# Optimization experiments

Hardware: AMD Instinct MI355X
Metric: run time of the kernel (lower is better)

## Reference

```python
import jax, jax.numpy as jnp
import numpy as np

N = 50000
E = 1600000
R = 4
D_IN = 128
D_OUT = 128


def setup_inputs() -> dict:
    key = jax.random.key(0)
    ks = jax.random.split(key, 7)
    x = jax.random.normal(ks[0], (N, D_IN), dtype=jnp.float32)
    vals = jax.random.normal(ks[1], (R, E), dtype=jnp.float32) * (1.0 / 32.0)
    weight = jax.random.normal(ks[2], (D_IN, D_OUT), dtype=jnp.float32) * (1.0 / np.sqrt(D_IN))
    filt = jax.random.uniform(ks[3], (R * N, 1), dtype=jnp.float32, minval=0.9, maxval=1.1)
    bias = jnp.zeros((D_OUT,), dtype=jnp.float32)
    rows = jax.random.randint(ks[4], (R, E), 0, N, dtype=jnp.int32)
    cols = jax.random.randint(ks[5], (R, E), 0, N, dtype=jnp.int32)
    return {"x": x, "vals": vals, "weight": weight, "filt": filt,
            "bias": bias, "rows": rows, "cols": cols}


def _spmm(rows, cols, vals, h, n):
    # sparse [n,n] @ dense [n,d] via gather + segment_sum
    return jax.ops.segment_sum(vals[:, None] * h[cols], rows, num_segments=n)


def reference(x, vals, weight, filt, bias, rows, cols):
    n = x.shape[0]
    h = x @ weight                                    # [N, out]
    # cat(d_list, dim=0) @ h  ->  stack of D_i @ h, i.e. [R, N, out]
    y = jax.vmap(lambda r, c, v: _spmm(r, c, v, h, n))(rows, cols, vals)
    y = filt.reshape(rows.shape[0], n, 1) * y         # elementwise wavelet filter
    # cat(d_list, dim=1) @ y  ->  sum_i D_i @ y_i
    out = jax.vmap(lambda r, c, v, yy: _spmm(r, c, v, yy, n))(rows, cols, vals, y).sum(axis=0)
    return out + bias
```

## Files before the change

### kernel.cpp

```cpp
#include <hip/hip_runtime.h>

#define N_NODES 50000
#define N_EDGES 1600000
#define R_WAV 4
#define D 128
#define NB 391
#define CHUNK 4096
#define NPBLK ((N_EDGES + CHUNK - 1) / CHUNK)
#define MAXB 4800

typedef unsigned int u32;
typedef unsigned short u16;

static __device__ inline u16 f2bf(float f) {
    u32 u = __float_as_uint(f);
    u = (u + 0x7FFFu + ((u >> 16) & 1u)) >> 16;
    return (u16)u;
}
static __device__ inline float bf_lo(u32 u) { return __uint_as_float(u << 16); }
static __device__ inline float bf_hi(u32 u) { return __uint_as_float(u & 0xFFFF0000u); }

__global__ __launch_bounds__(128) void gemm_xw(const float* __restrict__ x,
                                               const float* __restrict__ W,
                                               u16* __restrict__ h) {
    __shared__ float xs[4 * 128];
    const int j = threadIdx.x;
    const int row0 = blockIdx.x * 4;
    for (int t = j; t < 512; t += 128) xs[t] = x[(size_t)row0 * D + t];
    __syncthreads();
    float a0 = 0.f, a1 = 0.f, a2 = 0.f, a3 = 0.f;
#pragma unroll 8
    for (int k = 0; k < 128; ++k) {
        const float w = W[k * D + j];
        a0 += xs[k] * w;
        a1 += xs[128 + k] * w;
        a2 += xs[256 + k] * w;
        a3 += xs[384 + k] * w;
    }
    h[(size_t)(row0 + 0) * D + j] = f2bf(a0);
    h[(size_t)(row0 + 1) * D + j] = f2bf(a1);
    h[(size_t)(row0 + 2) * D + j] = f2bf(a2);
    h[(size_t)(row0 + 3) * D + j] = f2bf(a3);
}

__global__ __launch_bounds__(256) void bucket_hist_all(const int* __restrict__ rows_all,
                                                       int* __restrict__ cnt4) {
    __shared__ int lh[NB];
    const int r = blockIdx.y;
    const int* rows = rows_all + (size_t)r * N_EDGES;
    int* cnt = cnt4 + r * NB;
    const int tid = threadIdx.x;
    for (int i = tid; i < NB; i += 256) lh[i] = 0;
    __syncthreads();
    const int e0 = blockIdx.x * CHUNK;
    const int e1 = min(e0 + CHUNK, N_EDGES);
    for (int i = e0 + tid; i < e1; i += 256) atomicAdd(&lh[rows[i] >> 7], 1);
    __syncthreads();
    for (int i = tid; i < NB; i += 256) {
        const int c = lh[i];
        if (c) atomicAdd(&cnt[i], c);
    }
}

__global__ __launch_bounds__(512) void scan_buckets_all(const int* __restrict__ cnt4,
                                                        int* __restrict__ bptr4,
                                                        int* __restrict__ bcur4) {
    __shared__ int sa[512], sb[512];
    const int r = blockIdx.x;
    const int* cnt = cnt4 + r * NB;
    int* bptr = bptr4 + r * (NB + 1);
    int* bcur = bcur4 + r * NB;
    const int tid = threadIdx.x;
    const int v = (tid < NB) ? cnt[tid] : 0;
    sa[tid] = v;
    int* cur = sa;
    int* nxt = sb;
    for (int d = 1; d < 512; d <<= 1) {
        __syncthreads();
        int t = cur[tid];
        if (tid >= d) t += cur[tid - d];
        nxt[tid] = t;
        int* tmp = cur; cur = nxt; nxt = tmp;
    }
    __syncthreads();
    const int excl = cur[tid] - v;
    if (tid <= NB) bptr[tid] = excl;
    if (tid < NB) bcur[tid] = excl;
}

__global__ __launch_bounds__(256) void partition_kernel(const int* __restrict__ rows,
                                                        const int* __restrict__ cols,
                                                        const float* __restrict__ vals,
                                                        int* __restrict__ bcur,
                                                        int2* __restrict__ cv) {
    __shared__ int lh[NB], lptr[NB], lcur[NB], lbase[NB];
    __shared__ int sa[256], sb[256];
    __shared__ int2 st[CHUNK];
    const int tid = threadIdx.x;
    for (int i = tid; i < NB; i += 256) lh[i] = 0;
    __syncthreads();
    const int e0 = blockIdx.x * CHUNK;
    const int e1 = min(e0 + CHUNK, N_EDGES);
    const int cnt = e1 - e0;
    for (int i = e0 + tid; i < e1; i += 256) atomicAdd(&lh[rows[i] >> 7], 1);
    __syncthreads();
    const int p0 = (2 * tid < NB) ? lh[2 * tid] : 0;
    const int p1 = (2 * tid + 1 < NB) ? lh[2 * tid + 1] : 0;
    sa[tid] = p0 + p1;
    int* cur = sa;
    int* nxt = sb;
    for (int d = 1; d < 256; d <<= 1) {
        __syncthreads();
        int t = cur[tid];
        if (tid >= d) t += cur[tid - d];
        nxt[tid] = t;
        int* tmp = cur; cur = nxt; nxt = tmp;
    }
    __syncthreads();
    const int pe = cur[tid] - (p0 + p1);
    if (2 * tid < NB)     { lptr[2 * tid] = pe;           lcur[2 * tid] = pe; }
    if (2 * tid + 1 < NB) { lptr[2 * tid + 1] = pe + p0;  lcur[2 * tid + 1] = pe + p0; }
    __syncthreads();
    for (int i = e0 + tid; i < e1; i += 256) {
        const int row = rows[i];
        const int b = row >> 7;
        const int pos = atomicAdd(&lcur[b], 1);
        st[pos] = make_int2((int)(((u32)row << 16) | (u32)cols[i]), __float_as_int(vals[i]));
    }
    __syncthreads();
    for (int b = tid; b < NB; b += 256) {
        const int c = lh[b];
        int gb = 0;
        if (c) gb = atomicAdd(&bcur[b], c);
        lbase[b] = gb - lptr[b];
    }
    __syncthreads();
    for (int i = tid; i < cnt; i += 256) {
        const int2 e = st[i];
        const int b = (int)((u32)e.x >> 23);
        cv[lbase[b] + i] = e;
    }
}

__global__ __launch_bounds__(256) void bucket_csr(const int* __restrict__ bptr,
                                                  const int2* __restrict__ cv,
                                                  u32* __restrict__ cv4,
                                                  int* __restrict__ row_ptr) {
    __shared__ int lh[128], lexcl[128], lcur[128];
    __shared__ u32 st[MAXB];
    const int b = blockIdx.x;
    const int s = bptr[b], e1 = bptr[b + 1];
    const int cnt = e1 - s;
    const int tid = threadIdx.x;
    if (tid < 128) lh[tid] = 0;
    __syncthreads();
    for (int i = s + tid; i < e1; i += 256)
        atomicAdd(&lh[((u32)cv[i].x >> 16) & 127u], 1);
    __syncthreads();
    if (tid < 64) {
        const int p0 = lh[2 * tid], p1 = lh[2 * tid + 1];
        int ssum = p0 + p1;
#pragma unroll
        for (int d = 1; d < 64; d <<= 1) {
            const int t = __shfl_up(ssum, d, 64);
            if (tid >= d) ssum += t;
        }
        const int pe = ssum - (p0 + p1);
        lexcl[2 * tid] = pe;          lcur[2 * tid] = pe;
        lexcl[2 * tid + 1] = pe + p0; lcur[2 * tid + 1] = pe + p0;
    }
    __syncthreads();
    for (int i = s + tid; i < e1; i += 256) {
        const int2 E = cv[i];
        const int lr = (int)(((u32)E.x >> 16) & 127u);
        const int pos = atomicAdd(&lcur[lr], 1);
        if (pos < MAXB)
            st[pos] = ((u32)f2bf(__int_as_float(E.y)) << 16) | ((u32)E.x & 0xFFFFu);
    }
    __syncthreads();
    const int wb = (cnt < MAXB) ? cnt : MAXB;
    for (int i = tid; i < wb; i += 256) cv4[s + i] = st[i];
    if (tid < 128) {
        const int row = (b << 7) + tid;
        if (row < N_NODES) row_ptr[row] = s + lexcl[tid];
    }
    if (b == 0 && tid == 0) row_ptr[N_NODES] = N_EDGES;
}

__global__ __launch_bounds__(256) void spmm1(const int* __restrict__ row_ptr,
                                             const u32* __restrict__ cvp,
                                             const u32* __restrict__ h2,
                                             const float* __restrict__ filt_r,
                                             u32* __restrict__ y2) {
    const int row = __builtin_amdgcn_readfirstlane(blockIdx.x * 4 + (threadIdx.x >> 6));
    const int lane = threadIdx.x & 63;
    const int half = lane >> 5;
    const int l = lane & 31;
    int e = row_ptr[row];
    const int end = row_ptr[row + 1];
    float a0 = 0.f, a1 = 0.f, a2 = 0.f, a3 = 0.f;
    float b0 = 0.f, b1 = 0.f, b2 = 0.f, b3 = 0.f;
    for (; e + 8 <= end; e += 8) {
        const u32 c0 = cvp[e], c1 = cvp[e + 1], c2 = cvp[e + 2], c3 = cvp[e + 3];
        const u32 c4 = cvp[e + 4], c5 = cvp[e + 5], c6 = cvp[e + 6], c7 = cvp[e + 7];
        const u32 uA = half ? c1 : c0;
        const u32 uB = half ? c3 : c2;
        const u32 uC = half ? c5 : c4;
        const u32 uD = half ? c7 : c6;
        const uint2 gA = *(const uint2*)(h2 + (uA & 0xFFFFu) * 64 + 2 * l);
        const uint2 gB = *(const uint2*)(h2 + (uB & 0xFFFFu) * 64 + 2 * l);
        const uint2 gC = *(const uint2*)(h2 + (uC & 0xFFFFu) * 64 + 2 * l);
        const uint2 gD = *(const uint2*)(h2 + (uD & 0xFFFFu) * 64 + 2 * l);
        const float vA = __uint_as_float(uA & 0xFFFF0000u);
        const float vB = __uint_as_float(uB & 0xFFFF0000u);
        const float vC = __uint_as_float(uC & 0xFFFF0000u);
        const float vD = __uint_as_float(uD & 0xFFFF0000u);
        a0 += vA * bf_lo(gA.x); a1 += vA * bf_hi(gA.x);
        a2 += vA * bf_lo(gA.y); a3 += vA * bf_hi(gA.y);
        b0 += vB * bf_lo(gB.x); b1 += vB * bf_hi(gB.x);
        b2 += vB * bf_lo(gB.y); b3 += vB * bf_hi(gB.y);
        a0 += vC * bf_lo(gC.x); a1 += vC * bf_hi(gC.x);
        a2 += vC * bf_lo(gC.y); a3 += vC * bf_hi(gC.y);
        b0 += vD * bf_lo(gD.x); b1 += vD * bf_hi(gD.x);
        b2 += vD * bf_lo(gD.y); b3 += vD * bf_hi(gD.y);
    }
    for (; e < end; e += 2) {
        const u32 c0 = cvp[e];
        const u32 c1 = (e + 1 < end) ? cvp[e + 1] : 0u;
        const u32 uA = half ? c1 : c0;
        const uint2 gA = *(const uint2*)(h2 + (uA & 0xFFFFu) * 64 + 2 * l);
        const float vA = __uint_as_float(uA & 0xFFFF0000u);
        a0 += vA * bf_lo(gA.x); a1 += vA * bf_hi(gA.x);
        a2 += vA * bf_lo(gA.y); a3 += vA * bf_hi(gA.y);
    }
    a0 += b0; a1 += b1; a2 += b2; a3 += b3;
    a0 += __shfl_xor(a0, 32, 64);
    a1 += __shfl_xor(a1, 32, 64);
    a2 += __shfl_xor(a2, 32, 64);
    a3 += __shfl_xor(a3, 32, 64);
    const float f = filt_r[row];
    if (half == 0) {
        uint2 o;
        o.x = (u32)f2bf(f * a0) | ((u32)f2bf(f * a1) << 16);
        o.y = (u32)f2bf(f * a2) | ((u32)f2bf(f * a3) << 16);
        *(uint2*)(y2 + (size_t)row * 64 + 2 * l) = o;
    }
}

template <bool FIRST>
__global__ __launch_bounds__(256) void spmm2(const int* __restrict__ row_ptr,
                                             const u32* __restrict__ cvp,
                                             const u32* __restrict__ y2,
                                             const float* __restrict__ bias,
                                             float* __restrict__ out) {
    const int row = __builtin_amdgcn_readfirstlane(blockIdx.x * 4 + (threadIdx.x >> 6));
    const int lane = threadIdx.x & 63;
    const int half = lane >> 5;
    const int l = lane & 31;
    int e = row_ptr[row];
    const int end = row_ptr[row + 1];
    float a0 = 0.f, a1 = 0.f, a2 = 0.f, a3 = 0.f;
    float b0 = 0.f, b1 = 0.f, b2 = 0.f, b3 = 0.f;
    for (; e + 8 <= end; e += 8) {
        const u32 c0 = cvp[e], c1 = cvp[e + 1], c2 = cvp[e + 2], c3 = cvp[e + 3];
        const u32 c4 = cvp[e + 4], c5 = cvp[e + 5], c6 = cvp[e + 6], c7 = cvp[e + 7];
        const u32 uA = half ? c1 : c0;
        const u32 uB = half ? c3 : c2;
        const u32 uC = half ? c5 : c4;
        const u32 uD = half ? c7 : c6;
        const uint2 gA = *(const uint2*)(y2 + (uA & 0xFFFFu) * 64 + 2 * l);
        const uint2 gB = *(const uint2*)(y2 + (uB & 0xFFFFu) * 64 + 2 * l);
        const uint2 gC = *(const uint2*)(y2 + (uC & 0xFFFFu) * 64 + 2 * l);
        const uint2 gD = *(const uint2*)(y2 + (uD & 0xFFFFu) * 64 + 2 * l);
        const float vA = __uint_as_float(uA & 0xFFFF0000u);
        const float vB = __uint_as_float(uB & 0xFFFF0000u);
        const float vC = __uint_as_float(uC & 0xFFFF0000u);
        const float vD = __uint_as_float(uD & 0xFFFF0000u);
        a0 += vA * bf_lo(gA.x); a1 += vA * bf_hi(gA.x);
        a2 += vA * bf_lo(gA.y); a3 += vA * bf_hi(gA.y);
        b0 += vB * bf_lo(gB.x); b1 += vB * bf_hi(gB.x);
        b2 += vB * bf_lo(gB.y); b3 += vB * bf_hi(gB.y);
        a0 += vC * bf_lo(gC.x); a1 += vC * bf_hi(gC.x);
        a2 += vC * bf_lo(gC.y); a3 += vC * bf_hi(gC.y);
        b0 += vD * bf_lo(gD.x); b1 += vD * bf_hi(gD.x);
        b2 += vD * bf_lo(gD.y); b3 += vD * bf_hi(gD.y);
    }
    for (; e < end; e += 2) {
        const u32 c0 = cvp[e];
        const u32 c1 = (e + 1 < end) ? cvp[e + 1] : 0u;
        const u32 uA = half ? c1 : c0;
        const uint2 gA = *(const uint2*)(y2 + (uA & 0xFFFFu) * 64 + 2 * l);
        const float vA = __uint_as_float(uA & 0xFFFF0000u);
        a0 += vA * bf_lo(gA.x); a1 += vA * bf_hi(gA.x);
        a2 += vA * bf_lo(gA.y); a3 += vA * bf_hi(gA.y);
    }
    a0 += b0; a1 += b1; a2 += b2; a3 += b3;
    a0 += __shfl_xor(a0, 32, 64);
    a1 += __shfl_xor(a1, 32, 64);
    a2 += __shfl_xor(a2, 32, 64);
    a3 += __shfl_xor(a3, 32, 64);
    if (half == 0) {
        float* op = out + (size_t)row * D + 4 * l;
        if (FIRST) {
            const float4 bb = *(const float4*)(bias + 4 * l);
            *(float4*)op = make_float4(a0 + bb.x, a1 + bb.y, a2 + bb.z, a3 + bb.w);
        } else {
            const float4 cc = *(const float4*)op;
            *(float4*)op = make_float4(cc.x + a0, cc.y + a1, cc.z + a2, cc.w + a3);
        }
    }
}

extern "C" void kernel_launch(void* const* d_in, const int* in_sizes, int n_in,
                              void* d_out, int out_size, void* d_ws, size_t ws_size,
                              hipStream_t stream) {
    const float* x    = (const float*)d_in[0];
    const float* vals = (const float*)d_in[1];
    const float* W    = (const float*)d_in[2];
    const float* filt = (const float*)d_in[3];
    const float* bias = (const float*)d_in[4];
    const int*   rows = (const int*)d_in[5];
    const int*   cols = (const int*)d_in[6];
    float* out = (float*)d_out;

    char* ws = (char*)d_ws;
    u16*  h       = (u16*)(ws);
    u32*  y2      = (u32*)(ws + 12800000);
    int2* cv8     = (int2*)(ws + 25600000);
    u32*  cv4     = (u32*)(ws + 38400000);
    int*  row_ptr = (int*)(ws + 44800512);
    int*  cnt4    = (int*)(ws + 45000576);
    int*  bptr4   = (int*)(ws + 45006976);
    int*  bcur4   = (int*)(ws + 45013376);

    gemm_xw<<<N_NODES / 4, 128, 0, stream>>>(x, W, h);

    hipMemsetAsync(cnt4, 0, 4 * NB * sizeof(int), stream);
    bucket_hist_all<<<dim3(NPBLK, R_WAV), 256, 0, stream>>>(rows, cnt4);
    scan_buckets_all<<<R_WAV, 512, 0, stream>>>(cnt4, bptr4, bcur4);

    for (int r = 0; r < R_WAV; ++r) {
        const int*   rows_r = rows + (size_t)r * N_EDGES;
        const int*   cols_r = cols + (size_t)r * N_EDGES;
        const float* vals_r = vals + (size_t)r * N_EDGES;
        const float* filt_r = filt + (size_t)r * N_NODES;

        partition_kernel<<<NPBLK, 256, 0, stream>>>(rows_r, cols_r, vals_r,
                                                    bcur4 + r * NB, cv8);
        bucket_csr<<<NB, 256, 0, stream>>>(bptr4 + r * (NB + 1), cv8, cv4, row_ptr);
        spmm1<<<N_NODES / 4, 256, 0, stream>>>(row_ptr, cv4, (const u32*)h, filt_r, y2);
        if (r == 0)
            spmm2<true><<<N_NODES / 4, 256, 0, stream>>>(row_ptr, cv4, y2, bias, out);
        else
            spmm2<false><<<N_NODES / 4, 256, 0, stream>>>(row_ptr, cv4, y2, bias, out);
    }
}
```

Baseline: 734.2 us.

## Batch CSR build and first SpMM across wavelets; deterministic partition offsets

```diff
diff --git a/kernel.cpp b/kernel.cpp
--- a/kernel.cpp
+++ b/kernel.cpp
@@ -8,6 +8,7 @@
 #define CHUNK 4096
 #define NPBLK ((N_EDGES + CHUNK - 1) / CHUNK)
 #define MAXB 4800
+#define RP_STRIDE 50016
 
 typedef unsigned int u32;
 typedef unsigned short u16;
@@ -23,53 +24,74 @@
 __global__ __launch_bounds__(128) void gemm_xw(const float* __restrict__ x,
                                                const float* __restrict__ W,
                                                u16* __restrict__ h) {
-    __shared__ float xs[4 * 128];
     const int j = threadIdx.x;
-    const int row0 = blockIdx.x * 4;
-    for (int t = j; t < 512; t += 128) xs[t] = x[(size_t)row0 * D + t];
-    __syncthreads();
-    float a0 = 0.f, a1 = 0.f, a2 = 0.f, a3 = 0.f;
-#pragma unroll 8
+    const int row0 = blockIdx.x * 16;
+    const float* xr = x + (size_t)row0 * D;
+    float acc[16];
+#pragma unroll
+    for (int r = 0; r < 16; ++r) acc[r] = 0.f;
+#pragma unroll 4
     for (int k = 0; k < 128; ++k) {
         const float w = W[k * D + j];
-        a0 += xs[k] * w;
-        a1 += xs[128 + k] * w;
-        a2 += xs[256 + k] * w;
-        a3 += xs[384 + k] * w;
-    }
-    h[(size_t)(row0 + 0) * D + j] = f2bf(a0);
-    h[(size_t)(row0 + 1) * D + j] = f2bf(a1);
-    h[(size_t)(row0 + 2) * D + j] = f2bf(a2);
-    h[(size_t)(row0 + 3) * D + j] = f2bf(a3);
+#pragma unroll
+        for (int r = 0; r < 16; ++r) acc[r] += xr[r * D + k] * w;
+    }
+#pragma unroll
+    for (int r = 0; r < 16; ++r) h[(size_t)(row0 + r) * D + j] = f2bf(acc[r]);
 }
 
 __global__ __launch_bounds__(256) void bucket_hist_all(const int* __restrict__ rows_all,
-                                                       int* __restrict__ cnt4) {
+                                                       int* __restrict__ hist,
+                                                       int* __restrict__ deg) {
     __shared__ int lh[NB];
     const int r = blockIdx.y;
     const int* rows = rows_all + (size_t)r * N_EDGES;
-    int* cnt = cnt4 + r * NB;
+    int* dg = deg + (size_t)r * N_NODES;
     const int tid = threadIdx.x;
     for (int i = tid; i < NB; i += 256) lh[i] = 0;
     __syncthreads();
     const int e0 = blockIdx.x * CHUNK;
     const int e1 = min(e0 + CHUNK, N_EDGES);
-    for (int i = e0 + tid; i < e1; i += 256) atomicAdd(&lh[rows[i] >> 7], 1);
-    __syncthreads();
-    for (int i = tid; i < NB; i += 256) {
-        const int c = lh[i];
-        if (c) atomicAdd(&cnt[i], c);
-    }
+    for (int i = e0 + tid; i < e1; i += 256) {
+        const int row = rows[i];
+        atomicAdd(&lh[row >> 7], 1);
+        atomicAdd(&dg[row], 1);
+    }
+    __syncthreads();
+    int* hc = hist + ((size_t)r * NPBLK + blockIdx.x) * NB;
+    for (int i = tid; i < NB; i += 256) hc[i] = lh[i];
+}
+
+__global__ __launch_bounds__(512) void chunk_scan(const int* __restrict__ hist,
+                                                  int* __restrict__ chunkpre,
+                                                  int* __restrict__ cnt) {
+    __shared__ int sa[512], sb[512];
+    const int b = blockIdx.x;
+    const int r = blockIdx.y;
+    const int tid = threadIdx.x;
+    const int v = (tid < NPBLK) ? hist[((size_t)r * NPBLK + tid) * NB + b] : 0;
+    sa[tid] = v;
+    int* cur = sa;
+    int* nxt = sb;
+    for (int d = 1; d < 512; d <<= 1) {
+        __syncthreads();
+        int t = cur[tid];
+        if (tid >= d) t += cur[tid - d];
+        nxt[tid] = t;
+        int* tmp = cur; cur = nxt; nxt = tmp;
+    }
+    __syncthreads();
+    const int excl = cur[tid] - v;
+    if (tid < NPBLK) chunkpre[((size_t)r * NPBLK + tid) * NB + b] = excl;
+    if (tid == NPBLK - 1) cnt[r * NB + b] = excl + v;
 }
 
 __global__ __launch_bounds__(512) void scan_buckets_all(const int* __restrict__ cnt4,
-                                                        int* __restrict__ bptr4,
-                                                        int* __restrict__ bcur4) {
+                                                        int* __restrict__ bptr4) {
     __shared__ int sa[512], sb[512];
     const int r = blockIdx.x;
     const int* cnt = cnt4 + r * NB;
     int* bptr = bptr4 + r * (NB + 1);
-    int* bcur = bcur4 + r * NB;
     const int tid = threadIdx.x;
     const int v = (tid < NB) ? cnt[tid] : 0;
     sa[tid] = v;
@@ -85,25 +107,32 @@
     __syncthreads();
     const int excl = cur[tid] - v;
     if (tid <= NB) bptr[tid] = excl;
-    if (tid < NB) bcur[tid] = excl;
 }
 
 __global__ __launch_bounds__(256) void partition_kernel(const int* __restrict__ rows,
                                                         const int* __restrict__ cols,
                                                         const float* __restrict__ vals,
-                                                        int* __restrict__ bcur,
+                                                        const int* __restrict__ bptr_all,
+                                                        const int* __restrict__ chunkpre,
+                                                        const int* __restrict__ hist,
                                                         int2* __restrict__ cv) {
+    const int r = blockIdx.y;
+    rows += (size_t)r * N_EDGES;
+    cols += (size_t)r * N_EDGES;
+    vals += (size_t)r * N_EDGES;
+    cv   += (size_t)r * N_EDGES;
+    const int* bptr = bptr_all + r * (NB + 1);
+    const int* hc   = hist     + ((size_t)r * NPBLK + blockIdx.x) * NB;
+    const int* cp   = chunkpre + ((size_t)r * NPBLK + blockIdx.x) * NB;
     __shared__ int lh[NB], lptr[NB], lcur[NB], lbase[NB];
     __shared__ int sa[256], sb[256];
     __shared__ int2 st[CHUNK];
     const int tid = threadIdx.x;
-    for (int i = tid; i < NB; i += 256) lh[i] = 0;
+    for (int i = tid; i < NB; i += 256) lh[i] = hc[i];
     __syncthreads();
     const int e0 = blockIdx.x * CHUNK;
     const int e1 = min(e0 + CHUNK, N_EDGES);
     const int cnt = e1 - e0;
-    for (int i = e0 + tid; i < e1; i += 256) atomicAdd(&lh[rows[i] >> 7], 1);
-    __syncthreads();
     const int p0 = (2 * tid < NB) ? lh[2 * tid] : 0;
     const int p1 = (2 * tid + 1 < NB) ? lh[2 * tid + 1] : 0;
     sa[tid] = p0 + p1;
@@ -127,13 +156,7 @@
         const int pos = atomicAdd(&lcur[b], 1);
         st[pos] = make_int2((int)(((u32)row << 16) | (u32)cols[i]), __float_as_int(vals[i]));
     }
-    __syncthreads();
-    for (int b = tid; b < NB; b += 256) {
-        const int c = lh[b];
-        int gb = 0;
-        if (c) gb = atomicAdd(&bcur[b], c);
-        lbase[b] = gb - lptr[b];
-    }
+    for (int b = tid; b < NB; b += 256) lbase[b] = bptr[b] + cp[b] - lptr[b];
     __syncthreads();
     for (int i = tid; i < cnt; i += 256) {
         const int2 e = st[i];
@@ -142,23 +165,27 @@
     }
 }
 
-__global__ __launch_bounds__(256) void bucket_csr(const int* __restrict__ bptr,
+__global__ __launch_bounds__(256) void bucket_csr(const int* __restrict__ bptr_all,
+                                                  const int* __restrict__ deg,
                                                   const int2* __restrict__ cv,
                                                   u32* __restrict__ cv4,
                                                   int* __restrict__ row_ptr) {
-    __shared__ int lh[128], lexcl[128], lcur[128];
+    const int r = blockIdx.y;
+    const int* bptr = bptr_all + r * (NB + 1);
+    deg     += (size_t)r * N_NODES;
+    cv      += (size_t)r * N_EDGES;
+    cv4     += (size_t)r * N_EDGES;
+    row_ptr += r * RP_STRIDE;
+    __shared__ int lexcl[128], lcur[128];
     __shared__ u32 st[MAXB];
     const int b = blockIdx.x;
     const int s = bptr[b], e1 = bptr[b + 1];
     const int cnt = e1 - s;
     const int tid = threadIdx.x;
-    if (tid < 128) lh[tid] = 0;
-    __syncthreads();
-    for (int i = s + tid; i < e1; i += 256)
-        atomicAdd(&lh[((u32)cv[i].x >> 16) & 127u], 1);
-    __syncthreads();
     if (tid < 64) {
-        const int p0 = lh[2 * tid], p1 = lh[2 * tid + 1];
+        const int row0 = (b << 7) + 2 * tid;
+        const int p0 = (row0 < N_NODES) ? deg[row0] : 0;
+        const int p1 = (row0 + 1 < N_NODES) ? deg[row0 + 1] : 0;
         int ssum = p0 + p1;
 #pragma unroll
         for (int d = 1; d < 64; d <<= 1) {
@@ -184,14 +211,19 @@
         const int row = (b << 7) + tid;
         if (row < N_NODES) row_ptr[row] = s + lexcl[tid];
     }
-    if (b == 0 && tid == 0) row_ptr[N_NODES] = N_EDGES;
+    if (blockIdx.x == 0 && tid == 0) row_ptr[N_NODES] = N_EDGES;
 }
 
 __global__ __launch_bounds__(256) void spmm1(const int* __restrict__ row_ptr,
                                              const u32* __restrict__ cvp,
                                              const u32* __restrict__ h2,
-                                             const float* __restrict__ filt_r,
+                                             const float* __restrict__ filt,
                                              u32* __restrict__ y2) {
+    const int r = blockIdx.y;
+    row_ptr += r * RP_STRIDE;
+    cvp     += (size_t)r * N_EDGES;
+    filt    += (size_t)r * N_NODES;
+    y2      += (size_t)r * (N_NODES * 64);
     const int row = __builtin_amdgcn_readfirstlane(blockIdx.x * 4 + (threadIdx.x >> 6));
     const int lane = threadIdx.x & 63;
     const int half = lane >> 5;
@@ -200,6 +232,51 @@
     const int end = row_ptr[row + 1];
     float a0 = 0.f, a1 = 0.f, a2 = 0.f, a3 = 0.f;
     float b0 = 0.f, b1 = 0.f, b2 = 0.f, b3 = 0.f;
+    for (; e + 16 <= end; e += 16) {
+        u32 c[16];
+#pragma unroll
+        for (int i = 0; i < 16; ++i) c[i] = cvp[e + i];
+        const u32 u0 = half ? c[1] : c[0];
+        const u32 u1 = half ? c[3] : c[2];
+        const u32 u2 = half ? c[5] : c[4];
+        const u32 u3 = half ? c[7] : c[6];
+        const u32 u4 = half ? c[9] : c[8];
+        const u32 u5 = half ? c[11] : c[10];
+        const u32 u6 = half ? c[13] : c[12];
+        const u32 u7 = half ? c[15] : c[14];
+        const uint2 g0 = *(const uint2*)(h2 + (u0 & 0xFFFFu) * 64 + 2 * l);
+        const uint2 g1 = *(const uint2*)(h2 + (u1 & 0xFFFFu) * 64 + 2 * l);
+        const uint2 g2 = *(const uint2*)(h2 + (u2 & 0xFFFFu) * 64 + 2 * l);
+        const uint2 g3 = *(const uint2*)(h2 + (u3 & 0xFFFFu) * 64 + 2 * l);
+        const uint2 g4 = *(const uint2*)(h2 + (u4 & 0xFFFFu) * 64 + 2 * l);
+        const uint2 g5 = *(const uint2*)(h2 + (u5 & 0xFFFFu) * 64 + 2 * l);
+        const uint2 g6 = *(const uint2*)(h2 + (u6 & 0xFFFFu) * 64 + 2 * l);
+        const uint2 g7 = *(const uint2*)(h2 + (u7 & 0xFFFFu) * 64 + 2 * l);
+        const float v0 = __uint_as_float(u0 & 0xFFFF0000u);
+        const float v1 = __uint_as_float(u1 & 0xFFFF0000u);
+        const float v2 = __uint_as_float(u2 & 0xFFFF0000u);
+        const float v3 = __uint_as_float(u3 & 0xFFFF0000u);
+        const float v4 = __uint_as_float(u4 & 0xFFFF0000u);
+        const float v5 = __uint_as_float(u5 & 0xFFFF0000u);
+        const float v6 = __uint_as_float(u6 & 0xFFFF0000u);
+        const float v7 = __uint_as_float(u7 & 0xFFFF0000u);
+        a0 += v0 * bf_lo(g0.x); a1 += v0 * bf_hi(g0.x);
+        a2 += v0 * bf_lo(g0.y); a3 += v0 * bf_hi(g0.y);
+        b0 += v1 * bf_lo(g1.x); b1 += v1 * bf_hi(g1.x);
+        b2 += v1 * bf_lo(g1.y); b3 += v1 * bf_hi(g1.y);
+        a0 += v2 * bf_lo(g2.x); a1 += v2 * bf_hi(g2.x);
+        a2 += v2 * bf_lo(g2.y); a3 += v2 * bf_hi(g2.y);
+        b0 += v3 * bf_lo(g3.x); b1 += v3 * bf_hi(g3.x);
+        b2 += v3 * bf_lo(g3.y); b3 += v3 * bf_hi(g3.y);
+        a0 += v4 * bf_lo(g4.x); a1 += v4 * bf_hi(g4.x);
+        a2 += v4 * bf_lo(g4.y); a3 += v4 * bf_hi(g4.y);
+        b0 += v5 * bf_lo(g5.x); b1 += v5 * bf_hi(g5.x);
+        b2 += v5 * bf_lo(g5.y); b3 += v5 * bf_hi(g5.y);
+        a0 += v6 * bf_lo(g6.x); a1 += v6 * bf_hi(g6.x);
+        a2 += v6 * bf_lo(g6.y); a3 += v6 * bf_hi(g6.y);
+        b0 += v7 * bf_lo(g7.x); b1 += v7 * bf_hi(g7.x);
+        b2 += v7 * bf_lo(g7.y); b3 += v7 * bf_hi(g7.y);
+    }
     for (; e + 8 <= end; e += 8) {
         const u32 c0 = cvp[e], c1 = cvp[e + 1], c2 = cvp[e + 2], c3 = cvp[e + 3];
         const u32 c4 = cvp[e + 4], c5 = cvp[e + 5], c6 = cvp[e + 6], c7 = cvp[e + 7];
@@ -238,7 +315,7 @@
     a1 += __shfl_xor(a1, 32, 64);
     a2 += __shfl_xor(a2, 32, 64);
     a3 += __shfl_xor(a3, 32, 64);
-    const float f = filt_r[row];
+    const float f = filt[row];
     if (half == 0) {
         uint2 o;
         o.x = (u32)f2bf(f * a0) | ((u32)f2bf(f * a1) << 16);
@@ -261,6 +338,51 @@
     const int end = row_ptr[row + 1];
     float a0 = 0.f, a1 = 0.f, a2 = 0.f, a3 = 0.f;
     float b0 = 0.f, b1 = 0.f, b2 = 0.f, b3 = 0.f;
+    for (; e + 16 <= end; e += 16) {
+        u32 c[16];
+#pragma unroll
+        for (int i = 0; i < 16; ++i) c[i] = cvp[e + i];
+        const u32 u0 = half ? c[1] : c[0];
+        const u32 u1 = half ? c[3] : c[2];
+        const u32 u2 = half ? c[5] : c[4];
+        const u32 u3 = half ? c[7] : c[6];
+        const u32 u4 = half ? c[9] : c[8];
+        const u32 u5 = half ? c[11] : c[10];
+        const u32 u6 = half ? c[13] : c[12];
+        const u32 u7 = half ? c[15] : c[14];
+        const uint2 g0 = *(const uint2*)(y2 + (u0 & 0xFFFFu) * 64 + 2 * l);
+        const uint2 g1 = *(const uint2*)(y2 + (u1 & 0xFFFFu) * 64 + 2 * l);
+        const uint2 g2 = *(const uint2*)(y2 + (u2 & 0xFFFFu) * 64 + 2 * l);
+        const uint2 g3 = *(const uint2*)(y2 + (u3 & 0xFFFFu) * 64 + 2 * l);
+        const uint2 g4 = *(const uint2*)(y2 + (u4 & 0xFFFFu) * 64 + 2 * l);
+        const uint2 g5 = *(const uint2*)(y2 + (u5 & 0xFFFFu) * 64 + 2 * l);
+        const uint2 g6 = *(const uint2*)(y2 + (u6 & 0xFFFFu) * 64 + 2 * l);
+        const uint2 g7 = *(const uint2*)(y2 + (u7 & 0xFFFFu) * 64 + 2 * l);
+        const float v0 = __uint_as_float(u0 & 0xFFFF0000u);
+        const float v1 = __uint_as_float(u1 & 0xFFFF0000u);
+        const float v2 = __uint_as_float(u2 & 0xFFFF0000u);
+        const float v3 = __uint_as_float(u3 & 0xFFFF0000u);
+        const float v4 = __uint_as_float(u4 & 0xFFFF0000u);
+        const float v5 = __uint_as_float(u5 & 0xFFFF0000u);
+        const float v6 = __uint_as_float(u6 & 0xFFFF0000u);
+        const float v7 = __uint_as_float(u7 & 0xFFFF0000u);
+        a0 += v0 * bf_lo(g0.x); a1 += v0 * bf_hi(g0.x);
+        a2 += v0 * bf_lo(g0.y); a3 += v0 * bf_hi(g0.y);
+        b0 += v1 * bf_lo(g1.x); b1 += v1 * bf_hi(g1.x);
+        b2 += v1 * bf_lo(g1.y); b3 += v1 * bf_hi(g1.y);
+        a0 += v2 * bf_lo(g2.x); a1 += v2 * bf_hi(g2.x);
+        a2 += v2 * bf_lo(g2.y); a3 += v2 * bf_hi(g2.y);
+        b0 += v3 * bf_lo(g3.x); b1 += v3 * bf_hi(g3.x);
+        b2 += v3 * bf_lo(g3.y); b3 += v3 * bf_hi(g3.y);
+        a0 += v4 * bf_lo(g4.x); a1 += v4 * bf_hi(g4.x);
+        a2 += v4 * bf_lo(g4.y); a3 += v4 * bf_hi(g4.y);
+        b0 += v5 * bf_lo(g5.x); b1 += v5 * bf_hi(g5.x);
+        b2 += v5 * bf_lo(g5.y); b3 += v5 * bf_hi(g5.y);
+        a0 += v6 * bf_lo(g6.x); a1 += v6 * bf_hi(g6.x);
+        a2 += v6 * bf_lo(g6.y); a3 += v6 * bf_hi(g6.y);
+        b0 += v7 * bf_lo(g7.x); b1 += v7 * bf_hi(g7.x);
+        b2 += v7 * bf_lo(g7.y); b3 += v7 * bf_hi(g7.y);
+    }
     for (; e + 8 <= end; e += 8) {
         const u32 c0 = cvp[e], c1 = cvp[e + 1], c2 = cvp[e + 2], c3 = cvp[e + 3];
         const u32 c4 = cvp[e + 4], c5 = cvp[e + 5], c6 = cvp[e + 6], c7 = cvp[e + 7];
@@ -324,34 +446,37 @@
     float* out = (float*)d_out;
 
     char* ws = (char*)d_ws;
-    u16*  h       = (u16*)(ws);
-    u32*  y2      = (u32*)(ws + 12800000);
-    int2* cv8     = (int2*)(ws + 25600000);
-    u32*  cv4     = (u32*)(ws + 38400000);
-    int*  row_ptr = (int*)(ws + 44800512);
-    int*  cnt4    = (int*)(ws + 45000576);
-    int*  bptr4   = (int*)(ws + 45006976);
-    int*  bcur4   = (int*)(ws + 45013376);
-
-    gemm_xw<<<N_NODES / 4, 128, 0, stream>>>(x, W, h);
-
-    hipMemsetAsync(cnt4, 0, 4 * NB * sizeof(int), stream);
-    bucket_hist_all<<<dim3(NPBLK, R_WAV), 256, 0, stream>>>(rows, cnt4);
-    scan_buckets_all<<<R_WAV, 512, 0, stream>>>(cnt4, bptr4, bcur4);
-
+    u16*  h    = (u16*)(ws);
+    int*  deg  = (int*)(ws);
+    u32*  sh   = (u32*)(ws + 12800000);
+    int2* cv8  = (int2*)sh;
+    u32*  y2   = sh;
+    u32*  cv4  = (u32*)(ws + 64000000);
+    int*  hist = (int*)(ws + 64000000);
+    int*  cpre = (int*)(ws + 66446096);
+    int*  rp   = (int*)(ws + 89600000);
+    int*  cnt4 = (int*)(ws + 90400512);
+    int*  bptr4 = (int*)(ws + 90406768);
+
+    hipMemsetAsync(deg, 0, (size_t)R_WAV * N_NODES * sizeof(int), stream);
+    bucket_hist_all<<<dim3(NPBLK, R_WAV), 256, 0, stream>>>(rows, hist, deg);
+    chunk_scan<<<dim3(NB, R_WAV), 512, 0, stream>>>(hist, cpre, cnt4);
+    scan_buckets_all<<<R_WAV, 512, 0, stream>>>(cnt4, bptr4);
+    partition_kernel<<<dim3(NPBLK, R_WAV), 256, 0, stream>>>(rows, cols, vals,
+                                                             bptr4, cpre, hist, cv8);
+    bucket_csr<<<dim3(NB, R_WAV), 256, 0, stream>>>(bptr4, deg, cv8, cv4, rp);
+
+    gemm_xw<<<N_NODES / 16, 128, 0, stream>>>(x, W, h);
+
+    spmm1<<<dim3(N_NODES / 4, R_WAV), 256, 0, stream>>>(rp, cv4, (const u32*)h,
+                                                        filt, y2);
     for (int r = 0; r < R_WAV; ++r) {
-        const int*   rows_r = rows + (size_t)r * N_EDGES;
-        const int*   cols_r = cols + (size_t)r * N_EDGES;
-        const float* vals_r = vals + (size_t)r * N_EDGES;
-        const float* filt_r = filt + (size_t)r * N_NODES;
-
-        partition_kernel<<<NPBLK, 256, 0, stream>>>(rows_r, cols_r, vals_r,
-                                                    bcur4 + r * NB, cv8);
-        bucket_csr<<<NB, 256, 0, stream>>>(bptr4 + r * (NB + 1), cv8, cv4, row_ptr);
-        spmm1<<<N_NODES / 4, 256, 0, stream>>>(row_ptr, cv4, (const u32*)h, filt_r, y2);
+        const int* rp_r  = rp + r * RP_STRIDE;
+        const u32* cv4_r = cv4 + (size_t)r * N_EDGES;
+        const u32* y2_r  = y2 + (size_t)r * (N_NODES * 64);
         if (r == 0)
-            spmm2<true><<<N_NODES / 4, 256, 0, stream>>>(row_ptr, cv4, y2, bias, out);
+            spmm2<true><<<N_NODES / 4, 256, 0, stream>>>(rp_r, cv4_r, y2_r, bias, out);
         else
-            spmm2<false><<<N_NODES / 4, 256, 0, stream>>>(row_ptr, cv4, y2, bias, out);
-    }
-}
+            spmm2<false><<<N_NODES / 4, 256, 0, stream>>>(rp_r, cv4_r, y2_r, bias, out);
+    }
+}
```

Measured after the change: 926.4 us. 26.2% more time.
